# Kernel optimization log

Hardware: AMD Instinct MI355X
Metric: run time of the kernel (lower is better)

The kernel has to match this reference:

```python
import jax, jax.numpy as jnp
import numpy as np

NS, NV = 48, 10                    # scalar / vector multiplicities (cfg.ns, cfg.nv)
WN = NS * NS + NS * NV             # per-edge TP weight numel: paths 0e*0e->0e and 0e*1o->1o
OUT = NS + 3 * NV                  # out irreps 48x0e + 10x1o -> 78 dims
INV = float(1.0 / np.sqrt(NS))     # e3nn-style path normalization (fan_in = mul_in)
N_LIG, N_REC, N_ATOM = 2000, 2000, 15000
E_LL, E_RR, E_AA = 15000, 10000, 15000
E_LR, E_LA, E_AR = 5000, 8000, 8000


def setup_inputs() -> dict:
    key = jax.random.key(0)
    ks = jax.random.split(key, 40)
    f = lambda i, shape, s=1.0: jax.random.normal(ks[i], shape, dtype=jnp.float32) * s
    ii = lambda i, n, e: jax.random.randint(ks[i], (e,), 0, n, dtype=jnp.int32)
    w_s = (1.0 / (3 * NS)) ** 0.5
    return {
        'lig_x': f(0, (N_LIG, NS)), 'rec_x': f(1, (N_REC, NS)), 'atom_x': f(2, (N_ATOM, NS)),
        'll_attr': f(3, (E_LL, NS)), 'rr_attr': f(4, (E_RR, NS)), 'aa_attr': f(5, (E_AA, NS)),
        'lr_attr': f(6, (E_LR, NS)), 'la_attr': f(7, (E_LA, NS)), 'ar_attr': f(8, (E_AR, NS)),
        'll_sh': f(9, (E_LL, 9)), 'rr_sh': f(10, (E_RR, 9)), 'aa_sh': f(11, (E_AA, 9)),
        'lr_sh': f(12, (E_LR, 9)), 'la_sh': f(13, (E_LA, 9)), 'ar_sh': f(14, (E_AR, 9)),
        'mlp_w1': f(15, (9, 3 * NS, 3 * NS), w_s), 'mlp_b1': jnp.zeros((9, 3 * NS), jnp.float32),
        'mlp_w2': f(16, (9, 3 * NS, 3 * NS), w_s), 'mlp_b2': jnp.zeros((9, 3 * NS), jnp.float32),
        'mlp_w3': f(17, (9, 3 * NS, WN), w_s), 'mlp_b3': jnp.zeros((9, WN), jnp.float32),
        'll_src': ii(18, N_LIG, E_LL), 'll_dst': ii(19, N_LIG, E_LL),
        'rr_src': ii(20, N_REC, E_RR), 'rr_dst': ii(21, N_REC, E_RR),
        'aa_src': ii(22, N_ATOM, E_AA), 'aa_dst': ii(23, N_ATOM, E_AA),
        'lr_lig': ii(24, N_LIG, E_LR), 'lr_rec': ii(25, N_REC, E_LR),
        'la_lig': ii(26, N_LIG, E_LA), 'la_atom': ii(27, N_ATOM, E_LA),
        'ar_atom': ii(28, N_ATOM, E_AR), 'ar_rec': ii(29, N_REC, E_AR),
    }


def _tp_conv(src_x, dst_x, e_attr, e_sh, src_idx, dst_idx, n_dst, w1, b1, w2, b2, w3, b3):
    """FullyConnectedTensorProductConv: per-edge MLP -> TP weights, CG tensor
    product of gathered source features with edge SH, mean scatter to dst."""
    fs = src_x[src_idx]                                          # (E, ns) gather
    z = jnp.concatenate([e_attr, fs, dst_x[dst_idx]], axis=-1)
    h = jax.nn.relu(z @ w1 + b1)
    h = jax.nn.relu(h @ w2 + b2)
    w = h @ w3 + b3                                              # (E, WN) edge-conditioned TP weights
    w0 = w[:, : NS * NS].reshape(-1, NS, NS)                     # 0e x 0e -> 0e path
    wv = w[:, NS * NS :].reshape(-1, NS, NV)                     # 0e x 1o -> 1o path
    out0 = jnp.einsum('ei,eio->eo', fs, w0) * e_sh[:, :1] * INV  # (E, ns)
    outv = jnp.einsum('ei,eiv,em->evm', fs, wv, e_sh[:, 1:4]) * INV  # (E, nv, 3)
    msg = jnp.concatenate([out0, outv.reshape(-1, NV * 3)], axis=-1)
    agg = jax.ops.segment_sum(msg, dst_idx, num_segments=n_dst)
    deg = jax.ops.segment_sum(jnp.ones((msg.shape[0], 1), msg.dtype), dst_idx, num_segments=n_dst)
    return agg / jnp.maximum(deg, 1.0)                           # mean reduction


def reference(lig_x, rec_x, atom_x, ll_attr, rr_attr, aa_attr, lr_attr, la_attr, ar_attr,
              ll_sh, rr_sh, aa_sh, lr_sh, la_sh, ar_sh,
              mlp_w1, mlp_b1, mlp_w2, mlp_b2, mlp_w3, mlp_b3,
              ll_src, ll_dst, rr_src, rr_dst, aa_src, aa_dst,
              lr_lig, lr_rec, la_lig, la_atom, ar_atom, ar_rec):
    P = lambda c: (mlp_w1[c], mlp_b1[c], mlp_w2[c], mlp_b2[c], mlp_w3[c], mlp_b3[c])
    # one interaction layer = 9 structurally distinct convs (lig/rec/atom intra + 6 cross dirs)
    lig_u = (_tp_conv(lig_x, lig_x, ll_attr, ll_sh, ll_src, ll_dst, N_LIG, *P(0))
           + _tp_conv(rec_x, lig_x, lr_attr, lr_sh, lr_rec, lr_lig, N_LIG, *P(1))
           + _tp_conv(atom_x, lig_x, la_attr, la_sh, la_atom, la_lig, N_LIG, *P(2)))
    rec_u = (_tp_conv(lig_x, rec_x, lr_attr, lr_sh, lr_lig, lr_rec, N_REC, *P(3))
           + _tp_conv(rec_x, rec_x, rr_attr, rr_sh, rr_src, rr_dst, N_REC, *P(4))
           + _tp_conv(atom_x, rec_x, ar_attr, ar_sh, ar_atom, ar_rec, N_REC, *P(5)))
    atom_u = (_tp_conv(lig_x, atom_x, la_attr, la_sh, la_lig, la_atom, N_ATOM, *P(6))
            + _tp_conv(rec_x, atom_x, ar_attr, ar_sh, ar_rec, ar_atom, N_ATOM, *P(7))
            + _tp_conv(atom_x, atom_x, aa_attr, aa_sh, aa_src, aa_dst, N_ATOM, *P(8)))
    pad = lambda x: jnp.pad(x, ((0, 0), (0, OUT - NS)))          # residual: pad scalars to out irreps
    return jnp.concatenate([pad(lig_x) + lig_u, pad(rec_x) + rec_u, pad(atom_x) + atom_u], axis=0)
```

## Files before the change

kernel.cpp:

```cpp
#include <hip/hip_runtime.h>


namespace {

constexpr int NCONV = 9;
constexpr int ETOT  = 82000;
constexpr float INV = 0.14433756729740643f;

constexpr int EC[NCONV]     = {15000,5000,8000,5000,10000,8000,8000,8000,15000};
constexpr int NBLKC[NCONV]  = {118,40,63,40,79,63,63,63,118};
constexpr int EOFF[NCONV]   = {0,15000,20000,28000,33000,43000,51000,59000,67000};
constexpr int DEGOFF[NCONV] = {0,2000,4000,6000,8000,10000,12000,27000,42000};
constexpr int NODEC[NCONV]  = {2000,2000,2000,2000,2000,2000,15000,15000,15000};
constexpr int NBLK_TOT = 647;

typedef _Float16 f16;
typedef __attribute__((ext_vector_type(8))) _Float16 f16x8;
typedef __attribute__((ext_vector_type(4))) _Float16 f16x4;
typedef __attribute__((ext_vector_type(4))) float f32x4;

#define MFMA(a, b, c) __builtin_amdgcn_mfma_f32_16x16x32_f16((a), (b), (c), 0, 0, 0)

struct ConvPtrs {
  const float* src_x[NCONV];
  const float* dst_x[NCONV];
  const float* attr[NCONV];
  const float* sh[NCONV];
  const int*   sidx[NCONV];
  const int*   didx[NCONV];
};

}

__device__ __forceinline__ int xcd_remap(int bid) {
  const int xcd = bid & 7, slot = bid >> 3;
  return (xcd <= 6) ? (xcd * 81 + slot) : (567 + slot);
}

__device__ __forceinline__ int conv_decode(int bid, int& rem) {
  int c = 0; rem = bid;
  while (c < NCONV - 1 && rem >= NBLKC[c]) { rem -= NBLKC[c]; ++c; }
  return c;
}

__device__ __forceinline__ void gld_lds16(const void* g, void* l) {
  __builtin_amdgcn_global_load_lds(
      (const __attribute__((address_space(1))) void*)g,
      (__attribute__((address_space(3))) void*)l, 16, 0, 0);
}

__device__ __forceinline__ f32x4 cvt4(f16x4 h) {
  return (f32x4){(float)h[0], (float)h[1], (float)h[2], (float)h[3]};
}

__global__ __launch_bounds__(256) void prep_all(
    ConvPtrs P,
    const float* __restrict__ w1, const float* __restrict__ b1,
    const float* __restrict__ w2, const float* __restrict__ b2,
    const float* __restrict__ w3, const float* __restrict__ b3,
    f16* __restrict__ w1f, f16* __restrict__ w2f, f16* __restrict__ w3f,
    float* __restrict__ deg) {
  __shared__ float W[145][60];
  const int blk = blockIdx.x;
  if (blk < 203) {
    const int unit = blk * 4 + (threadIdx.x >> 6);
    if (unit >= 810) return;
    const int l = threadIdx.x & 63;
    const int sel = unit >= 405, bb = sel ? unit - 405 : unit;
    const int c = bb / 45, r2 = bb % 45, cb = r2 / 5, s = r2 % 5;
    const float* w  = sel ? w2 : w1;
    const float* bi = sel ? b2 : b1;
    f16* dst = (sel ? w2f : w1f) + ((size_t)(c * 9 + cb) * 5 + s) * 512;
    const int n = cb * 16 + (l & 15);
    f16x8 pack;
#pragma unroll
    for (int j = 0; j < 8; ++j) {
      const int k = s * 32 + ((l >> 4) << 3) + j;
      float v = 0.f;
      if (k < 144)       v = w[((size_t)c * 144 + k) * 144 + n];
      else if (k == 144) v = bi[c * 144 + n];
      pack[j] = (f16)v;
    }
    ((f16x8*)dst)[l] = pack;
  } else if (blk < 635) {
    const int b = blk - 203;
    const int c = b / 48, i = b % 48;
    const float* wc = w3 + (size_t)c * 144 * 2784;
    const float* bc = b3 + (size_t)c * 2784;
    for (int u = threadIdx.x; u < 145 * 58; u += 256) {
      const int row = u / 58, t = u - row * 58;
      const int col = (t < 48) ? (i * 48 + t) : (2304 + i * 10 + (t - 48));
      const float* src = (row == 144) ? bc : (wc + (size_t)row * 2784);
      W[row][t] = src[col];
    }
    __syncthreads();
    f16* dst = w3f + (size_t)(c * 48 + i) * 20 * 512;
#pragma unroll 1
    for (int it = 0; it < 40; ++it) {
      const int f = it * 256 + threadIdx.x;
      const int s = f >> 11, g2 = f & 2047, cb = g2 >> 9, l = (g2 >> 3) & 63, j = f & 7;
      const int k = s * 32 + ((l >> 4) << 3) + j;
      const int col = cb * 16 + (l & 15);
      const float v = (k <= 144 && col < 58) ? W[k][col] : 0.f;
      dst[f] = (f16)v;
    }
  } else {
    const int gid = (blk - 635) * 256 + threadIdx.x;
    if (gid >= ETOT) return;
    int c = 0;
    while (c < NCONV - 1 && gid >= EOFF[c + 1]) ++c;
    const int e = gid - EOFF[c];
    atomicAdd(&deg[DEGOFF[c] + P.didx[c][e]], 1.0f);
  }
}

__global__ __launch_bounds__(256) void scan_kernel(
    const float* __restrict__ deg, int* __restrict__ offs, int* __restrict__ cursor) {
  __shared__ int part[256];
  const int c = blockIdx.x, N = NODEC[c], base = DEGOFF[c];
  const int tid = threadIdx.x;
  const int chunk = (N + 255) / 256;
  const int start = tid * chunk;
  const int end = (start + chunk < N) ? (start + chunk) : N;
  int s = 0;
  for (int i = start; i < end; ++i) s += (int)deg[base + i];
  part[tid] = s;
  __syncthreads();
  if (tid == 0) {
    int acc = 0;
    for (int k = 0; k < 256; ++k) { int t = part[k]; part[k] = acc; acc += t; }
  }
  __syncthreads();
  int acc = part[tid];
  for (int i = start; i < end; ++i) {
    offs[base + i] = acc; cursor[base + i] = acc;
    acc += (int)deg[base + i];
  }
}

__global__ __launch_bounds__(256) void slot_kernel(
    ConvPtrs P, int* __restrict__ cursor, int* __restrict__ inv_slot) {
  const int gid = blockIdx.x * 256 + threadIdx.x;
  if (gid >= ETOT) return;
  int c = 0;
  while (c < NCONV - 1 && gid >= EOFF[c + 1]) ++c;
  const int e = gid - EOFF[c];
  const int d = P.didx[c][e];
  inv_slot[gid] = atomicAdd(&cursor[DEGOFF[c] + d], 1);
}

template<int NCB, int CB0>
__device__ __forceinline__ void layer_mm(
    const f16x8* __restrict__ Av, const f16x8* __restrict__ wv,
    int c, int lane, int wr, f32x4 acc[4][5]) {
#pragma unroll
  for (int rb = 0; rb < 4; ++rb)
#pragma unroll
    for (int cb = 0; cb < NCB; ++cb) acc[rb][cb] = (f32x4)0.0f;
#pragma unroll
  for (int s = 0; s < 5; ++s) {
    f16x8 B[NCB];
#pragma unroll
    for (int cb = 0; cb < NCB; ++cb)
      B[cb] = wv[((size_t)(c * 9 + CB0 + cb) * 5 + s) * 64 + lane];
    f16x8 A[4];
#pragma unroll
    for (int rb = 0; rb < 4; ++rb) A[rb] = Av[((wr * 4 + rb) * 5 + s) * 64 + lane];
#pragma unroll
    for (int rb = 0; rb < 4; ++rb)
#pragma unroll
      for (int cb = 0; cb < NCB; ++cb)
        acc[rb][cb] = MFMA(A[rb], B[cb], acc[rb][cb]);
  }
}

template<int NCB, int CB0>
__device__ __forceinline__ void layer_wb(const f32x4 acc[4][5], f16* __restrict__ At,
                                         int lane, int wr) {
#pragma unroll
  for (int cb = 0; cb < NCB; ++cb) {
    const int k = (CB0 + cb) * 16 + (lane & 15);
    const int s = k >> 5, g = (k >> 3) & 3, j = k & 7;
#pragma unroll
    for (int rb = 0; rb < 4; ++rb)
#pragma unroll
      for (int r = 0; r < 4; ++r) {
        const int row = ((lane >> 4) << 2) + r;
        At[((((wr * 4 + rb) * 5 + s) * 4 + g) * 16 + row) * 8 + j] =
            (f16)fmaxf(acc[rb][cb][r], 0.f);
      }
  }
}

__global__ __launch_bounds__(256, 3) void mlp_kernel(
    ConvPtrs P, const f16* __restrict__ w1f, const f16* __restrict__ w2f,
    f16* __restrict__ h2g, f16* __restrict__ fstg) {
  __shared__ __align__(16) char smem[54272];
  f16* Atile = (f16*)smem;
  f16 (*fst)[128] = (f16 (*)[128])(smem + 40960);
  int* sidb = (int*)(smem + 53248);
  int* dstb = (int*)(smem + 53760);

  const int f = xcd_remap(blockIdx.x);
  int rem; const int c = conv_decode(f, rem);
  const int E = EC[c], e0 = rem * 128;
  const int tid = threadIdx.x, lane = tid & 63, w = tid >> 6;
  const int wr = w >> 1, wc = w & 1;

  if (tid < 128) {
    int ec = e0 + tid; if (ec >= E) ec = E - 1;
    sidb[tid] = P.sidx[c][ec];
    dstb[tid] = P.didx[c][ec];
  }
  __syncthreads();

  {
    const float* attr = P.attr[c];
    const float* sx = P.src_x[c];
    const float* dx = P.dst_x[c];
#pragma unroll
    for (int it = 0; it < 10; ++it) {
      const int u = it * 256 + tid, j8 = u >> 7, e = u & 127;
      int ec = e0 + e; if (ec >= E) ec = E - 1;
      const float* p;
      if (j8 < 6)       p = attr + (size_t)ec * 48 + j8 * 8;
      else if (j8 < 12) p = sx + (size_t)sidb[e] * 48 + (j8 - 6) * 8;
      else if (j8 < 18) p = dx + (size_t)dstb[e] * 48 + (j8 - 12) * 8;
      else              p = attr;
      const f32x4 va = *(const f32x4*)p;
      const f32x4 vb = *(const f32x4*)(p + 4);
      float v[8];
#pragma unroll
      for (int t = 0; t < 4; ++t) { v[t] = va[t]; v[4 + t] = vb[t]; }
      if (j8 == 18) {
        v[0] = 1.f;
#pragma unroll
        for (int t = 1; t < 8; ++t) v[t] = 0.f;
      } else if (j8 == 19) {
#pragma unroll
        for (int t = 0; t < 8; ++t) v[t] = 0.f;
      }
      f16x8 h;
#pragma unroll
      for (int t = 0; t < 8; ++t) h[t] = (f16)v[t];
      if (j8 >= 6 && j8 < 12) {
#pragma unroll
        for (int t = 0; t < 8; ++t) fst[(j8 - 6) * 8 + t][e] = h[t];
      }
      const int s = j8 >> 2, g = j8 & 3, rbg = e >> 4, row = e & 15;
      ((f16x8*)Atile)[((rbg * 5 + s) * 4 + g) * 16 + row] = h;
    }
  }
  __syncthreads();

  const f16x8* Av = (const f16x8*)Atile;
  f32x4 acc[4][5];
  if (wc == 0) layer_mm<5, 0>(Av, (const f16x8*)w1f, c, lane, wr, acc);
  else         layer_mm<4, 5>(Av, (const f16x8*)w1f, c, lane, wr, acc);
  __syncthreads();
  if (wc == 0) layer_wb<5, 0>(acc, Atile, lane, wr);
  else         layer_wb<4, 5>(acc, Atile, lane, wr);
  __syncthreads();
  if (wc == 0) layer_mm<5, 0>(Av, (const f16x8*)w2f, c, lane, wr, acc);
  else         layer_mm<4, 5>(Av, (const f16x8*)w2f, c, lane, wr, acc);
  __syncthreads();
  if (wc == 0) layer_wb<5, 0>(acc, Atile, lane, wr);
  else         layer_wb<4, 5>(acc, Atile, lane, wr);
  __syncthreads();

  const f16x8* As = (const f16x8*)Atile;
  f16x8* hd = (f16x8*)(h2g + (size_t)f * 20480);
#pragma unroll
  for (int t = 0; t < 10; ++t) hd[t * 256 + tid] = As[t * 256 + tid];
  const f16x8* fs8 = (const f16x8*)fst;
  f16x8* fd = (f16x8*)(fstg + (size_t)f * 6144);
#pragma unroll
  for (int t = 0; t < 3; ++t) fd[t * 256 + tid] = fs8[t * 256 + tid];
}

__device__ __forceinline__ void bilin_step(
    const f16* __restrict__ slot, const f16 (*fstl)[128], int i,
    const f16x8 Af[4][5], f32x4 msg[4][2], int lane, int wr, int wc) {
  f16x4 fsh[4];
#pragma unroll
  for (int rb = 0; rb < 4; ++rb)
    fsh[rb] = *(const f16x4*)&fstl[i][wr * 64 + rb * 16 + ((lane >> 4) << 2)];
  const f16x8* bv = (const f16x8*)slot;
  __builtin_amdgcn_s_setprio(1);
#pragma unroll
  for (int cb = 0; cb < 2; ++cb) {
    f16x8 Bf[5];
#pragma unroll
    for (int s = 0; s < 5; ++s) Bf[s] = bv[(s * 4 + wc * 2 + cb) * 64 + lane];
    f32x4 T[4];
#pragma unroll
    for (int rb = 0; rb < 4; ++rb) T[rb] = (f32x4)0.0f;
#pragma unroll
    for (int s = 0; s < 5; ++s)
#pragma unroll
      for (int rb = 0; rb < 4; ++rb) T[rb] = MFMA(Af[rb][s], Bf[s], T[rb]);
#pragma unroll
    for (int rb = 0; rb < 4; ++rb) msg[rb][cb] += cvt4(fsh[rb]) * T[rb];
  }
  __builtin_amdgcn_s_setprio(0);
}

__global__ __launch_bounds__(256, 3) void bilin_kernel(
    ConvPtrs P, const f16* __restrict__ w3f, const f16* __restrict__ h2g,
    const f16* __restrict__ fstg, const float* __restrict__ deg,
    const int* __restrict__ inv_slot, f16* __restrict__ medge) {
  __shared__ __align__(16) char smem[53248];
  f16* ring = (f16*)smem;
  f16 (*fstl)[128] = (f16 (*)[128])(smem + 40960);

  const int f = xcd_remap(blockIdx.x);
  int rem; const int c = conv_decode(f, rem);
  const int E = EC[c], e0 = rem * 128;
  const int tid = threadIdx.x, lane = tid & 63, w = tid >> 6;
  const int wr = w >> 1, wc = w & 1;

  const f16x8* hv = (const f16x8*)(h2g + (size_t)f * 20480);
  f16x8 Af[4][5];
#pragma unroll
  for (int rb = 0; rb < 4; ++rb)
#pragma unroll
    for (int s = 0; s < 5; ++s)
      Af[rb][s] = hv[((wr * 4 + rb) * 5 + s) * 64 + lane];

  const f16* fsrc = fstg + (size_t)f * 6144;
#pragma unroll
  for (int t = 0; t < 3; ++t) {
    const int chunk = w * 3 + t;
    gld_lds16(fsrc + chunk * 512 + lane * 8, ((f16*)fstl) + chunk * 512);
  }
  const f16* __restrict__ w3c = w3f + (size_t)(c * 48) * 10240;
#pragma unroll
  for (int q = 0; q < 5; ++q) {
    const int chunk = q * 4 + w;
    gld_lds16(w3c + chunk * 512 + lane * 8, ring + chunk * 512);
  }

  f32x4 msg[4][2];
#pragma unroll
  for (int rb = 0; rb < 4; ++rb)
#pragma unroll
    for (int cb = 0; cb < 2; ++cb) msg[rb][cb] = (f32x4)0.0f;

#pragma unroll 1
  for (int i = 0; i < 47; ++i) {
    __builtin_amdgcn_s_barrier();
    const f16* gsrc = w3c + (size_t)(i + 1) * 10240;
    f16* bdst = ring + ((i + 1) & 1) * 10240;
#pragma unroll
    for (int q = 0; q < 5; ++q) {
      const int chunk = q * 4 + w;
      gld_lds16(gsrc + chunk * 512 + lane * 8, bdst + chunk * 512);
    }
    asm volatile("s_waitcnt vmcnt(5)" ::: "memory");
    __builtin_amdgcn_s_barrier();
    __builtin_amdgcn_sched_barrier(0);
    bilin_step(ring + (i & 1) * 10240, fstl, i, Af, msg, lane, wr, wc);
  }
  __builtin_amdgcn_s_barrier();
  asm volatile("s_waitcnt vmcnt(0)" ::: "memory");
  __builtin_amdgcn_s_barrier();
  bilin_step(ring + (47 & 1) * 10240, fstl, 47, Af, msg, lane, wr, wc);

  const float* __restrict__ shp = P.sh[c];
  const float* __restrict__ degc = deg + DEGOFF[c];
  const int* __restrict__ didx = P.didx[c];
#pragma unroll
  for (int rb = 0; rb < 4; ++rb)
#pragma unroll
    for (int r = 0; r < 4; ++r) {
      const int el = wr * 64 + rb * 16 + ((lane >> 4) << 2) + r;
      const int ec = e0 + el;
      if (ec >= E) continue;
      const float sc = INV / fmaxf(degc[didx[ec]], 1.f);
      const float* shq = shp + (size_t)ec * 9;
      const float s0 = shq[0], s1 = shq[1], s2 = shq[2], s3 = shq[3];
      const int pos = inv_slot[EOFF[c] + ec];
      f16* mp = medge + (size_t)(EOFF[c] + pos) * 80;
#pragma unroll
      for (int cb = 0; cb < 2; ++cb) {
        const int col = (wc * 2 + cb) * 16 + (lane & 15);
        const float v = msg[rb][cb][r] * sc;
        if (col < 48) {
          mp[col] = (f16)(v * s0);
        } else if (col < 58) {
          const int vv = col - 48;
          mp[48 + vv * 3 + 0] = (f16)(v * s1);
          mp[48 + vv * 3 + 1] = (f16)(v * s2);
          mp[48 + vv * 3 + 2] = (f16)(v * s3);
        }
      }
    }
}

__global__ __launch_bounds__(256) void finalize_kernel(
    const float* __restrict__ lig, const float* __restrict__ rec,
    const float* __restrict__ atom, const int* __restrict__ offs,
    const int* __restrict__ cursor, const f16* __restrict__ medge,
    float* __restrict__ out) {
  const int tid = threadIdx.x;
  if (tid >= 240) return;
  const int r3 = tid / 80, j = tid - r3 * 80;
  const int row = blockIdx.x * 3 + r3;
  if (row >= 19000 || j >= 78) return;
  int node, cb; const float* x;
  if (row < 2000)      { node = row;        cb = 0; x = lig; }
  else if (row < 4000) { node = row - 2000; cb = 3; x = rec; }
  else                 { node = row - 4000; cb = 6; x = atom; }
  float r = (j < 48) ? x[(size_t)node * 48 + j] : 0.f;
#pragma unroll
  for (int t = 0; t < 3; ++t) {
    const int c = cb + t;
    const int base = DEGOFF[c] + node;
    const int o = offs[base], e = cursor[base];
    for (int k = o; k < e; ++k)
      r += (float)medge[(size_t)(EOFF[c] + k) * 80 + j];
  }
  out[(size_t)row * 78 + j] = r;
}

extern "C" void kernel_launch(void* const* d_in, const int* in_sizes, int n_in,
                              void* d_out, int out_size, void* d_ws, size_t ws_size,
                              hipStream_t stream) {
  (void)in_sizes; (void)n_in; (void)out_size; (void)ws_size;
  const float* lig_x  = (const float*)d_in[0];
  const float* rec_x  = (const float*)d_in[1];
  const float* atom_x = (const float*)d_in[2];
  const float* attr_ll = (const float*)d_in[3];
  const float* attr_rr = (const float*)d_in[4];
  const float* attr_aa = (const float*)d_in[5];
  const float* attr_lr = (const float*)d_in[6];
  const float* attr_la = (const float*)d_in[7];
  const float* attr_ar = (const float*)d_in[8];
  const float* sh_ll = (const float*)d_in[9];
  const float* sh_rr = (const float*)d_in[10];
  const float* sh_aa = (const float*)d_in[11];
  const float* sh_lr = (const float*)d_in[12];
  const float* sh_la = (const float*)d_in[13];
  const float* sh_ar = (const float*)d_in[14];
  const float* w1 = (const float*)d_in[15];
  const float* b1 = (const float*)d_in[16];
  const float* w2 = (const float*)d_in[17];
  const float* b2 = (const float*)d_in[18];
  const float* w3 = (const float*)d_in[19];
  const float* b3 = (const float*)d_in[20];
  const int* ll_src = (const int*)d_in[21];
  const int* ll_dst = (const int*)d_in[22];
  const int* rr_src = (const int*)d_in[23];
  const int* rr_dst = (const int*)d_in[24];
  const int* aa_src = (const int*)d_in[25];
  const int* aa_dst = (const int*)d_in[26];
  const int* lr_lig = (const int*)d_in[27];
  const int* lr_rec = (const int*)d_in[28];
  const int* la_lig = (const int*)d_in[29];
  const int* la_atom = (const int*)d_in[30];
  const int* ar_atom = (const int*)d_in[31];
  const int* ar_rec  = (const int*)d_in[32];

  f16* w1f = (f16*)d_ws;
  f16* w2f = w1f + 207360;
  f16* w3f = w2f + 207360;
  float* deg     = (float*)(w3f + 4423680);
  int*   offs    = (int*)(deg + 57000);
  int*   cursor  = offs + 57000;
  int*   inv_slot= cursor + 57000;
  f16*   medge   = (f16*)(inv_slot + 82000);
  f16*   h2g     = medge + 6560000;
  f16*   fstg    = h2g + 13250560;

  ConvPtrs P;
  const float* SX[NCONV] = {lig_x, rec_x, atom_x, lig_x, rec_x, atom_x, lig_x, rec_x, atom_x};
  const float* DX[NCONV] = {lig_x, lig_x, lig_x, rec_x, rec_x, rec_x, atom_x, atom_x, atom_x};
  const float* AT[NCONV] = {attr_ll, attr_lr, attr_la, attr_lr, attr_rr, attr_ar, attr_la, attr_ar, attr_aa};
  const float* SH[NCONV] = {sh_ll, sh_lr, sh_la, sh_lr, sh_rr, sh_ar, sh_la, sh_ar, sh_aa};
  const int*   SI[NCONV] = {ll_src, lr_rec, la_atom, lr_lig, rr_src, ar_atom, la_lig, ar_rec, aa_src};
  const int*   DI[NCONV] = {ll_dst, lr_lig, la_lig, lr_rec, rr_dst, ar_rec, la_atom, ar_atom, aa_dst};
  for (int cc = 0; cc < NCONV; ++cc) {
    P.src_x[cc] = SX[cc]; P.dst_x[cc] = DX[cc]; P.attr[cc] = AT[cc];
    P.sh[cc] = SH[cc]; P.sidx[cc] = SI[cc]; P.didx[cc] = DI[cc];
  }

  hipMemsetAsync(deg, 0, 57000 * sizeof(float), stream);
  prep_all<<<956, 256, 0, stream>>>(P, w1, b1, w2, b2, w3, b3, w1f, w2f, w3f, deg);
  scan_kernel<<<NCONV, 256, 0, stream>>>(deg, offs, cursor);
  slot_kernel<<<(ETOT + 255) / 256, 256, 0, stream>>>(P, cursor, inv_slot);
  mlp_kernel<<<NBLK_TOT, 256, 0, stream>>>(P, w1f, w2f, h2g, fstg);
  bilin_kernel<<<NBLK_TOT, 256, 0, stream>>>(P, w3f, h2g, fstg, deg, inv_slot, medge);
  finalize_kernel<<<(19000 + 2) / 3, 256, 0, stream>>>(lig_x, rec_x, atom_x, offs,
                                                       cursor, medge, (float*)d_out);
}
```

Measured before the change: 192.8 us.

## Fuse MLP and bilinear kernels and merge scan with slot assignment

The MLP kernel and the bilinear tensor-product kernel are merged into one kernel, so the hidden activations and gathered source features stay in LDS and registers instead of going through global scratch buffers (h2g, fstg). The LDS A-tile is reused as the double-buffered ring for the w3 weights once the activations have been loaded into registers. The scan and slot-assignment kernels are also merged into one 9-block launch that does the per-conv atomics serially. This removes two launches and a large global round trip, but the slot atomics now run on only 9 blocks, and register pressure in the fused kernel may grow.

```diff
diff --git a/kernel.cpp b/kernel.cpp
--- a/kernel.cpp
+++ b/kernel.cpp
@@ -114,8 +114,9 @@
   }
 }
 
-__global__ __launch_bounds__(256) void scan_kernel(
-    const float* __restrict__ deg, int* __restrict__ offs, int* __restrict__ cursor) {
+__global__ __launch_bounds__(256) void scan_slot(
+    ConvPtrs P, const float* __restrict__ deg, int* __restrict__ offs,
+    int* __restrict__ cursor, int* __restrict__ inv_slot) {
   __shared__ int part[256];
   const int c = blockIdx.x, N = NODEC[c], base = DEGOFF[c];
   const int tid = threadIdx.x;
@@ -136,17 +137,11 @@
     offs[base + i] = acc; cursor[base + i] = acc;
     acc += (int)deg[base + i];
   }
-}
-
-__global__ __launch_bounds__(256) void slot_kernel(
-    ConvPtrs P, int* __restrict__ cursor, int* __restrict__ inv_slot) {
-  const int gid = blockIdx.x * 256 + threadIdx.x;
-  if (gid >= ETOT) return;
-  int c = 0;
-  while (c < NCONV - 1 && gid >= EOFF[c + 1]) ++c;
-  const int e = gid - EOFF[c];
-  const int d = P.didx[c][e];
-  inv_slot[gid] = atomicAdd(&cursor[DEGOFF[c] + d], 1);
+  __syncthreads();
+  const int E = EC[c];
+  const int* __restrict__ didx = P.didx[c];
+  for (int e = tid; e < E; e += 256)
+    inv_slot[EOFF[c] + e] = atomicAdd(&cursor[base + didx[e]], 1);
 }
 
 template<int NCB, int CB0>
@@ -192,9 +187,37 @@
   }
 }
 
-__global__ __launch_bounds__(256, 3) void mlp_kernel(
+__device__ __forceinline__ void bilin_step(
+    const f16* __restrict__ slot, const f16 (*fstl)[128], int i,
+    const f16x8 Af[4][5], f32x4 msg[4][2], int lane, int wr, int wc) {
+  f16x4 fsh[4];
+#pragma unroll
+  for (int rb = 0; rb < 4; ++rb)
+    fsh[rb] = *(const f16x4*)&fstl[i][wr * 64 + rb * 16 + ((lane >> 4) << 2)];
+  const f16x8* bv = (const f16x8*)slot;
+  __builtin_amdgcn_s_setprio(1);
+#pragma unroll
+  for (int cb = 0; cb < 2; ++cb) {
+    f16x8 Bf[5];
+#pragma unroll
+    for (int s = 0; s < 5; ++s) Bf[s] = bv[(s * 4 + wc * 2 + cb) * 64 + lane];
+    f32x4 T[4];
+#pragma unroll
+    for (int rb = 0; rb < 4; ++rb) T[rb] = (f32x4)0.0f;
+#pragma unroll
+    for (int s = 0; s < 5; ++s)
+#pragma unroll
+      for (int rb = 0; rb < 4; ++rb) T[rb] = MFMA(Af[rb][s], Bf[s], T[rb]);
+#pragma unroll
+    for (int rb = 0; rb < 4; ++rb) msg[rb][cb] += cvt4(fsh[rb]) * T[rb];
+  }
+  __builtin_amdgcn_s_setprio(0);
+}
+
+__global__ __launch_bounds__(256, 3) void fused_conv(
     ConvPtrs P, const f16* __restrict__ w1f, const f16* __restrict__ w2f,
-    f16* __restrict__ h2g, f16* __restrict__ fstg) {
+    const f16* __restrict__ w3f, const float* __restrict__ deg,
+    const int* __restrict__ inv_slot, f16* __restrict__ medge) {
   __shared__ __align__(16) char smem[54272];
   f16* Atile = (f16*)smem;
   f16 (*fst)[128] = (f16 (*)[128])(smem + 40960);
@@ -268,71 +291,15 @@
   else         layer_wb<4, 5>(acc, Atile, lane, wr);
   __syncthreads();
 
-  const f16x8* As = (const f16x8*)Atile;
-  f16x8* hd = (f16x8*)(h2g + (size_t)f * 20480);
-#pragma unroll
-  for (int t = 0; t < 10; ++t) hd[t * 256 + tid] = As[t * 256 + tid];
-  const f16x8* fs8 = (const f16x8*)fst;
-  f16x8* fd = (f16x8*)(fstg + (size_t)f * 6144);
-#pragma unroll
-  for (int t = 0; t < 3; ++t) fd[t * 256 + tid] = fs8[t * 256 + tid];
-}
-
-__device__ __forceinline__ void bilin_step(
-    const f16* __restrict__ slot, const f16 (*fstl)[128], int i,
-    const f16x8 Af[4][5], f32x4 msg[4][2], int lane, int wr, int wc) {
-  f16x4 fsh[4];
+  f16x8 Af[4][5];
 #pragma unroll
   for (int rb = 0; rb < 4; ++rb)
-    fsh[rb] = *(const f16x4*)&fstl[i][wr * 64 + rb * 16 + ((lane >> 4) << 2)];
-  const f16x8* bv = (const f16x8*)slot;
-  __builtin_amdgcn_s_setprio(1);
-#pragma unroll
-  for (int cb = 0; cb < 2; ++cb) {
-    f16x8 Bf[5];
-#pragma unroll
-    for (int s = 0; s < 5; ++s) Bf[s] = bv[(s * 4 + wc * 2 + cb) * 64 + lane];
-    f32x4 T[4];
-#pragma unroll
-    for (int rb = 0; rb < 4; ++rb) T[rb] = (f32x4)0.0f;
 #pragma unroll
     for (int s = 0; s < 5; ++s)
-#pragma unroll
-      for (int rb = 0; rb < 4; ++rb) T[rb] = MFMA(Af[rb][s], Bf[s], T[rb]);
-#pragma unroll
-    for (int rb = 0; rb < 4; ++rb) msg[rb][cb] += cvt4(fsh[rb]) * T[rb];
-  }
-  __builtin_amdgcn_s_setprio(0);
-}
-
-__global__ __launch_bounds__(256, 3) void bilin_kernel(
-    ConvPtrs P, const f16* __restrict__ w3f, const f16* __restrict__ h2g,
-    const f16* __restrict__ fstg, const float* __restrict__ deg,
-    const int* __restrict__ inv_slot, f16* __restrict__ medge) {
-  __shared__ __align__(16) char smem[53248];
-  f16* ring = (f16*)smem;
-  f16 (*fstl)[128] = (f16 (*)[128])(smem + 40960);
-
-  const int f = xcd_remap(blockIdx.x);
-  int rem; const int c = conv_decode(f, rem);
-  const int E = EC[c], e0 = rem * 128;
-  const int tid = threadIdx.x, lane = tid & 63, w = tid >> 6;
-  const int wr = w >> 1, wc = w & 1;
-
-  const f16x8* hv = (const f16x8*)(h2g + (size_t)f * 20480);
-  f16x8 Af[4][5];
-#pragma unroll
-  for (int rb = 0; rb < 4; ++rb)
-#pragma unroll
-    for (int s = 0; s < 5; ++s)
-      Af[rb][s] = hv[((wr * 4 + rb) * 5 + s) * 64 + lane];
-
-  const f16* fsrc = fstg + (size_t)f * 6144;
-#pragma unroll
-  for (int t = 0; t < 3; ++t) {
-    const int chunk = w * 3 + t;
-    gld_lds16(fsrc + chunk * 512 + lane * 8, ((f16*)fstl) + chunk * 512);
-  }
+      Af[rb][s] = Av[((wr * 4 + rb) * 5 + s) * 64 + lane];
+  __syncthreads();
+
+  f16* ring = Atile;
   const f16* __restrict__ w3c = w3f + (size_t)(c * 48) * 10240;
 #pragma unroll
   for (int q = 0; q < 5; ++q) {
@@ -359,12 +326,12 @@
     asm volatile("s_waitcnt vmcnt(5)" ::: "memory");
     __builtin_amdgcn_s_barrier();
     __builtin_amdgcn_sched_barrier(0);
-    bilin_step(ring + (i & 1) * 10240, fstl, i, Af, msg, lane, wr, wc);
+    bilin_step(ring + (i & 1) * 10240, fst, i, Af, msg, lane, wr, wc);
   }
   __builtin_amdgcn_s_barrier();
   asm volatile("s_waitcnt vmcnt(0)" ::: "memory");
   __builtin_amdgcn_s_barrier();
-  bilin_step(ring + (47 & 1) * 10240, fstl, 47, Af, msg, lane, wr, wc);
+  bilin_step(ring + (47 & 1) * 10240, fst, 47, Af, msg, lane, wr, wc);
 
   const float* __restrict__ shp = P.sh[c];
   const float* __restrict__ degc = deg + DEGOFF[c];
@@ -469,8 +436,6 @@
   int*   cursor  = offs + 57000;
   int*   inv_slot= cursor + 57000;
   f16*   medge   = (f16*)(inv_slot + 82000);
-  f16*   h2g     = medge + 6560000;
-  f16*   fstg    = h2g + 13250560;
 
   ConvPtrs P;
   const float* SX[NCONV] = {lig_x, rec_x, atom_x, lig_x, rec_x, atom_x, lig_x, rec_x, atom_x};
@@ -486,10 +451,8 @@
 
   hipMemsetAsync(deg, 0, 57000 * sizeof(float), stream);
   prep_all<<<956, 256, 0, stream>>>(P, w1, b1, w2, b2, w3, b3, w1f, w2f, w3f, deg);
-  scan_kernel<<<NCONV, 256, 0, stream>>>(deg, offs, cursor);
-  slot_kernel<<<(ETOT + 255) / 256, 256, 0, stream>>>(P, cursor, inv_slot);
-  mlp_kernel<<<NBLK_TOT, 256, 0, stream>>>(P, w1f, w2f, h2g, fstg);
-  bilin_kernel<<<NBLK_TOT, 256, 0, stream>>>(P, w3f, h2g, fstg, deg, inv_slot, medge);
+  scan_slot<<<NCONV, 256, 0, stream>>>(P, deg, offs, cursor, inv_slot);
+  fused_conv<<<NBLK_TOT, 256, 0, stream>>>(P, w1f, w2f, w3f, deg, inv_slot, medge);
   finalize_kernel<<<(19000 + 2) / 3, 256, 0, stream>>>(lig_x, rec_x, atom_x, offs,
                                                        cursor, medge, (float*)d_out);
 }
```

Result: slower. 252.0 us (+30.7%).
